# Kernel tuning notes

Measured on AMD Instinct MI355X. Metric: run time of the kernel, lower is better.

Reference implementation:

```python
import jax, jax.numpy as jnp
import numpy as np

# ---- structural constants (mirror e3nn SO3.tensor_productRs bookkeeping) ----
MUL = 2                      # multiplicity of every irrep in Rs_in / Rs_out
LS = [0, 1, 2]               # irrep orders present in Rs_in and Rs_out
L_MAX = 2                    # spherical-harmonics cutoff -> Y_dim = 9
N_BASIS, HIDDEN = 64, 64     # radial model sizes
R_MAX, GAMMA = 3.5, 4.0      # gaussian radial basis params


def _filter_paths():
    """One entry (l_filter) per (mul_out, mul_in, l_in, l_out, l_f) path."""
    paths = []
    for l_in in LS:
        for l_out in LS:
            for lf in range(abs(l_in - l_out), min(l_in + l_out, L_MAX) + 1):
                paths.extend([lf] * (MUL * MUL))  # mul_in * mul_out copies
    return paths  # len == n_path == 60


def _build_mix_matrices():
    """rf_mix[K, n_path]: broadcast each radial path weight over its 2l+1 components.
    ylm_mix[K, 9]: select Y_{l,m} for each filter component. Both 0/1, block sparse."""
    paths = _filter_paths()
    n_path = len(paths)
    K = sum(2 * l + 1 for l in paths)          # 204
    y_off = {0: 0, 1: 1, 2: 4}                 # offset of l-block inside Y (dim 9)
    rf = np.zeros((K, n_path), dtype=np.float32)
    ylm = np.zeros((K, 9), dtype=np.float32)
    k = 0
    for p, l in enumerate(paths):
        for m in range(2 * l + 1):
            rf[k, p] = 1.0
            ylm[k, y_off[l] + m] = 1.0
            k += 1
    return rf, ylm, n_path, K


def _sh_l012(n):
    """Real spherical harmonics l=0..2 on unit vectors n[Z,3] -> Y[9, Z]."""
    x, y, z = n[:, 0], n[:, 1], n[:, 2]
    c0 = 0.28209479177387814   # 1/(2 sqrt(pi))
    c1 = 0.4886025119029199    # sqrt(3/(4 pi))
    c2a = 1.0925484305920792   # sqrt(15/(4 pi))
    c2b = 0.31539156525252005  # sqrt(5/(16 pi))
    c2c = 0.5462742152960396   # sqrt(15/(16 pi))
    one = jnp.ones_like(x)
    return jnp.stack([
        c0 * one,
        c1 * y, c1 * z, c1 * x,
        c2a * x * y, c2a * y * z, c2b * (3.0 * z * z - 1.0), c2a * x * z,
        c2c * (x * x - y * y),
    ], axis=0)


def setup_inputs() -> dict:
    key = jax.random.key(0)
    k_r, k_cg, k_w1, k_w2 = jax.random.split(key, 4)
    Z = 65536
    D = MUL * sum(2 * l + 1 for l in LS)       # 18 (dim_in == dim_out)
    rf_np, ylm_np, n_path, K = _build_mix_matrices()
    r = 2.0 * jax.random.normal(k_r, (Z, 3), dtype=jnp.float32)
    cg = jax.random.normal(k_cg, (K, D, D), dtype=jnp.float32) / np.sqrt(K)
    W1 = jax.random.normal(k_w1, (N_BASIS, HIDDEN), dtype=jnp.float32) / np.sqrt(N_BASIS)
    b1 = jnp.zeros((HIDDEN,), dtype=jnp.float32)
    W2 = jax.random.normal(k_w2, (HIDDEN, n_path), dtype=jnp.float32) / np.sqrt(HIDDEN)
    b2 = jnp.zeros((n_path,), dtype=jnp.float32)
    return {"r": r, "W1": W1, "b1": b1, "W2": W2, "b2": b2,
            "cg": cg, "rf_mix": jnp.asarray(rf_np), "ylm_mix": jnp.asarray(ylm_np)}


def reference(r, W1, b1, W2, b2, cg, rf_mix, ylm_mix):
    radii = jnp.linalg.norm(r, axis=1)                    # [Z]
    n = r / (radii[:, None] + 1e-12)                      # unit directions
    Y = _sh_l012(n)                                       # [9, Z]  (sh returns [m, ...])
    centers = jnp.linspace(0.0, R_MAX, N_BASIS, dtype=jnp.float32)
    B = jnp.exp(-GAMMA * (radii[:, None] - centers) ** 2) # gaussian radial basis [Z, 64]
    R = jax.nn.relu(B @ W1 + b1) @ W2 + b2                # RadialModel -> [Z, n_path]
    Rm = jnp.einsum('kp,zp->zk', rf_mix, R)               # 'ij,zj->zi'
    Ym = jnp.einsum('ky,yz->zk', ylm_mix, Y)              # 'ij,jz->zi'
    # 'kij,zk,zk->zij' : fuse the two per-point vectors, then one GEMM over k
    kernel = jnp.einsum('kij,zk->zij', cg, Rm * Ym)       # [Z, 18, 18]
    return kernel
```

## Files before the change

### kernel.cpp

```cpp
#include <hip/hip_runtime.h>

#define NPATH 60
#define KDIM  204
#define KPAD  224
#define NIJ   324
#define NTIL  21
#define HID   64

#define BHS   88
#define CLS   232

typedef short bf16x8 __attribute__((ext_vector_type(8)));
typedef float f32x4  __attribute__((ext_vector_type(4)));

__device__ __align__(16) unsigned short g_w1s[4096];
__device__ __align__(16) unsigned short g_w2s[4096];
__device__ __align__(16) unsigned short g_cgs[75264];
__device__ unsigned char g_ptab[KDIM];
__device__ unsigned char g_ytab[KDIM];

__device__ inline unsigned short f2bf(float f) {
    unsigned int u = __builtin_bit_cast(unsigned int, f);
    u += 0x7fffu + ((u >> 16) & 1u);
    return (unsigned short)(u >> 16);
}
__device__ inline float bf2f(unsigned short h) {
    unsigned int u = ((unsigned int)h) << 16;
    return __builtin_bit_cast(float, u);
}

__global__ void prep_kernel(const float* __restrict__ W1, const float* __restrict__ W2,
                            const float* __restrict__ cg, const float* __restrict__ rf,
                            const float* __restrict__ ylm)
{
    int idx = blockIdx.x * 256 + threadIdx.x;
    if (idx < 4096) {
        int e = idx & 7, ln = (idx >> 3) & 63, nt = (idx >> 9) & 3, kc = idx >> 11;
        int k = kc * 32 + (ln >> 4) * 8 + e;
        int n = nt * 16 + (ln & 15);
        g_w1s[idx] = f2bf(W1[k * HID + n]);
    } else if (idx < 8192) {
        int j = idx - 4096;
        int e = j & 7, ln = (j >> 3) & 63, nt = (j >> 9) & 3, kc = j >> 11;
        int k = kc * 32 + (ln >> 4) * 8 + e;
        int n = nt * 16 + (ln & 15);
        g_w2s[j] = f2bf(n < NPATH ? W2[k * NPATH + n] : 0.0f);
    } else if (idx < 8192 + 75264) {
        int j = idx - 8192;
        int e = j & 7, ln = (j >> 3) & 63;
        int nt = (j >> 9) % NTIL;
        int kc = j / (512 * NTIL);
        int k = kc * 32 + (ln >> 4) * 8 + e;
        int n = nt * 16 + (ln & 15);
        g_cgs[j] = f2bf((k < KDIM && n < NIJ) ? cg[k * NIJ + n] : 0.0f);
    } else if (idx < 8192 + 75264 + KDIM) {
        int k = idx - (8192 + 75264);
        int p = 0, yy = 0;
        for (int q = 0; q < NPATH; q++) if (rf[k * NPATH + q] != 0.0f) p = q;
        for (int q = 0; q < 9; q++)     if (ylm[k * 9 + q]   != 0.0f) yy = q;
        g_ptab[k] = (unsigned char)p;
        g_ytab[k] = (unsigned char)yy;
    }
}

union SmemU {
    struct {
        unsigned short Blds[64][BHS];
        unsigned short Hlds[64][BHS];
    } p1;
    unsigned short Clds[64][CLS];
};

__global__ __launch_bounds__(256) void fused_kernel(
    const float* __restrict__ r, const float* __restrict__ b1,
    const float* __restrict__ b2, float* __restrict__ out)
{
    __shared__ SmemU sm;
    __shared__ unsigned short Rl[64][61];
    __shared__ float Yl[64][9];
    __shared__ unsigned char ptabL[KDIM];
    __shared__ unsigned char ytabL[KDIM];

    const int tid  = threadIdx.x;
    const int wv   = tid >> 6;
    const int lane = tid & 63;
    const int quad = lane >> 4;
    const int l16  = lane & 15;
    const int z0   = blockIdx.x * 64;

    for (int k = tid; k < KDIM; k += 256) {
        ptabL[k] = g_ptab[k];
        ytabL[k] = g_ytab[k];
    }
    if (tid < 64) {
        int z = z0 + tid;
        float x = r[z * 3 + 0], y = r[z * 3 + 1], zc = r[z * 3 + 2];
        float rad = sqrtf(x * x + y * y + zc * zc);
        float inv = 1.0f / (rad + 1e-12f);
        float nx = x * inv, ny = y * inv, nz = zc * inv;
        const float c0 = 0.28209479177387814f, c1 = 0.4886025119029199f;
        const float c2a = 1.0925484305920792f, c2b = 0.31539156525252005f, c2c = 0.5462742152960396f;
        Yl[tid][0] = c0;
        Yl[tid][1] = c1 * ny;
        Yl[tid][2] = c1 * nz;
        Yl[tid][3] = c1 * nx;
        Yl[tid][4] = c2a * nx * ny;
        Yl[tid][5] = c2a * ny * nz;
        Yl[tid][6] = c2b * (3.0f * nz * nz - 1.0f);
        Yl[tid][7] = c2a * nx * nz;
        Yl[tid][8] = c2c * (nx * nx - ny * ny);
    }
    {
        int zz = tid >> 2, grp = tid & 3;
        int z = z0 + zz;
        float x = r[z * 3 + 0], y = r[z * 3 + 1], zc = r[z * 3 + 2];
        float rad = sqrtf(x * x + y * y + zc * zc);
        const float step = 3.5f / 63.0f;
        const float NL2E = -5.770780163555852f;
        unsigned int* dst = (unsigned int*)&sm.p1.Blds[zz][grp * 16];
        #pragma unroll
        for (int ii = 0; ii < 8; ii++) {
            int i0 = grp * 16 + ii * 2;
            float d0 = rad - (float)i0 * step;
            float d1 = rad - (float)(i0 + 1) * step;
            unsigned int u0 = f2bf(__builtin_amdgcn_exp2f(d0 * d0 * NL2E));
            unsigned int u1 = f2bf(__builtin_amdgcn_exp2f(d1 * d1 * NL2E));
            dst[ii] = u0 | (u1 << 16);
        }
    }
    __syncthreads();

    {
        bf16x8 a0 = *(const bf16x8*)&sm.p1.Blds[wv * 16 + l16][0 + quad * 8];
        bf16x8 a1 = *(const bf16x8*)&sm.p1.Blds[wv * 16 + l16][32 + quad * 8];
        #pragma unroll
        for (int nt = 0; nt < 4; nt++) {
            bf16x8 bb0 = *(const bf16x8*)&g_w1s[((0 * 4 + nt) * 64 + lane) * 8];
            bf16x8 bb1 = *(const bf16x8*)&g_w1s[((1 * 4 + nt) * 64 + lane) * 8];
            f32x4 acc = {0.f, 0.f, 0.f, 0.f};
            acc = __builtin_amdgcn_mfma_f32_16x16x32_bf16(a0, bb0, acc, 0, 0, 0);
            acc = __builtin_amdgcn_mfma_f32_16x16x32_bf16(a1, bb1, acc, 0, 0, 0);
            int h = nt * 16 + l16;
            float bias = b1[h];
            #pragma unroll
            for (int rr = 0; rr < 4; rr++) {
                float v = acc[rr] + bias;
                v = v > 0.0f ? v : 0.0f;
                sm.p1.Hlds[wv * 16 + quad * 4 + rr][h] = f2bf(v);
            }
        }
    }
    __syncthreads();

    {
        bf16x8 a0 = *(const bf16x8*)&sm.p1.Hlds[wv * 16 + l16][0 + quad * 8];
        bf16x8 a1 = *(const bf16x8*)&sm.p1.Hlds[wv * 16 + l16][32 + quad * 8];
        #pragma unroll
        for (int nt = 0; nt < 4; nt++) {
            bf16x8 bb0 = *(const bf16x8*)&g_w2s[((0 * 4 + nt) * 64 + lane) * 8];
            bf16x8 bb1 = *(const bf16x8*)&g_w2s[((1 * 4 + nt) * 64 + lane) * 8];
            f32x4 acc = {0.f, 0.f, 0.f, 0.f};
            acc = __builtin_amdgcn_mfma_f32_16x16x32_bf16(a0, bb0, acc, 0, 0, 0);
            acc = __builtin_amdgcn_mfma_f32_16x16x32_bf16(a1, bb1, acc, 0, 0, 0);
            int p = nt * 16 + l16;
            if (p < NPATH) {
                float bias = b2[p];
                #pragma unroll
                for (int rr = 0; rr < 4; rr++)
                    Rl[wv * 16 + quad * 4 + rr][p] = f2bf(acc[rr] + bias);
            }
        }
    }
    __syncthreads();

    for (int idx = tid; idx < 64 * (KPAD / 2); idx += 256) {
        int z = idx / (KPAD / 2);
        int k = (idx % (KPAD / 2)) * 2;
        unsigned int u = 0;
        if (k < KDIM) {
            float cA = bf2f(Rl[z][ptabL[k]])     * Yl[z][ytabL[k]];
            float cB = bf2f(Rl[z][ptabL[k + 1]]) * Yl[z][ytabL[k + 1]];
            u = (unsigned int)f2bf(cA) | ((unsigned int)f2bf(cB) << 16);
        }
        *(unsigned int*)&sm.Clds[z][k] = u;
    }
    __syncthreads();

    const int ntb = wv * 5 + (wv > 0 ? 1 : 0);
    const int cnt = (wv == 0) ? 6 : 5;

    f32x4 acc[6][4];
    #pragma unroll
    for (int i = 0; i < 6; i++)
        #pragma unroll
        for (int zt = 0; zt < 4; zt++)
            acc[i][zt] = (f32x4){0.f, 0.f, 0.f, 0.f};

    #pragma unroll
    for (int kc = 0; kc < 7; kc++) {
        bf16x8 az[4];
        #pragma unroll
        for (int zt = 0; zt < 4; zt++)
            az[zt] = *(const bf16x8*)&sm.Clds[zt * 16 + l16][kc * 32 + quad * 8];

        bf16x8 bg[6];
        #pragma unroll
        for (int i = 0; i < 6; i++) {
            int nt = ntb + i; if (nt > NTIL - 1) nt = NTIL - 1;
            bg[i] = *(const bf16x8*)&g_cgs[((kc * NTIL + nt) * 64 + lane) * 8];
        }
        #pragma unroll
        for (int i = 0; i < 6; i++) {
            if (i < cnt) {
                #pragma unroll
                for (int zt = 0; zt < 4; zt++)
                    acc[i][zt] = __builtin_amdgcn_mfma_f32_16x16x32_bf16(az[zt], bg[i], acc[i][zt], 0, 0, 0);
            }
        }
    }

    #pragma unroll
    for (int i = 0; i < 6; i++) {
        if (i < cnt) {
            int col = (ntb + i) * 16 + l16;
            if (col < NIJ) {
                #pragma unroll
                for (int zt = 0; zt < 4; zt++) {
                    #pragma unroll
                    for (int rr = 0; rr < 4; rr++)
                        out[(z0 + zt * 16 + quad * 4 + rr) * NIJ + col] = acc[i][zt][rr];
                }
            }
        }
    }
}

extern "C" void kernel_launch(void* const* d_in, const int* in_sizes, int n_in,
                              void* d_out, int out_size, void* d_ws, size_t ws_size,
                              hipStream_t stream) {
    const float* r   = (const float*)d_in[0];
    const float* W1  = (const float*)d_in[1];
    const float* b1  = (const float*)d_in[2];
    const float* W2  = (const float*)d_in[3];
    const float* b2  = (const float*)d_in[4];
    const float* cg  = (const float*)d_in[5];
    const float* rf  = (const float*)d_in[6];
    const float* ylm = (const float*)d_in[7];
    float* out = (float*)d_out;

    const int Z = in_sizes[0] / 3;

    prep_kernel<<<327, 256, 0, stream>>>(W1, W2, cg, rf, ylm);
    fused_kernel<<<Z / 64, 256, 0, stream>>>(r, b1, b2, out);
}
```

Baseline: 139.4 us.

## Swizzle C tile in LDS, pack index tables, split output GEMM into halves

Packs the path and Y index tables into one 32-bit word per pair of k values. The C-building loop now gives each lane one z row and sweeps k, so the table lookups become wave-uniform. The C tile in LDS is written and read with an XOR swizzle on the byte offset to avoid bank conflicts on the bf16x8 reads. The output GEMM is split into two halves of 3 n-tiles each, which cuts live accumulator registers and lets the first half's stores overlap the second half's compute, at the cost of reloading the A fragments from LDS twice.

Measured after the change: 139.4 us. Within noise of the previous version (-0.0%).

```diff
diff --git a/kernel.cpp b/kernel.cpp
--- a/kernel.cpp
+++ b/kernel.cpp
@@ -16,8 +16,7 @@
 __device__ __align__(16) unsigned short g_w1s[4096];
 __device__ __align__(16) unsigned short g_w2s[4096];
 __device__ __align__(16) unsigned short g_cgs[75264];
-__device__ unsigned char g_ptab[KDIM];
-__device__ unsigned char g_ytab[KDIM];
+__device__ unsigned int  g_pyk[112];
 
 __device__ inline unsigned short f2bf(float f) {
     unsigned int u = __builtin_bit_cast(unsigned int, f);
@@ -53,13 +52,17 @@
         int k = kc * 32 + (ln >> 4) * 8 + e;
         int n = nt * 16 + (ln & 15);
         g_cgs[j] = f2bf((k < KDIM && n < NIJ) ? cg[k * NIJ + n] : 0.0f);
-    } else if (idx < 8192 + 75264 + KDIM) {
-        int k = idx - (8192 + 75264);
-        int p = 0, yy = 0;
-        for (int q = 0; q < NPATH; q++) if (rf[k * NPATH + q] != 0.0f) p = q;
-        for (int q = 0; q < 9; q++)     if (ylm[k * 9 + q]   != 0.0f) yy = q;
-        g_ptab[k] = (unsigned char)p;
-        g_ytab[k] = (unsigned char)yy;
+    } else if (idx < 8192 + 75264 + 112) {
+        int j = idx - (8192 + 75264);
+        int k0 = 2 * j, k1 = 2 * j + 1;
+        unsigned p0 = 0, y0 = 0, p1 = 0, y1 = 0;
+        if (k0 < KDIM) {
+            for (int q = 0; q < NPATH; q++) if (rf[k0 * NPATH + q] != 0.0f) p0 = q;
+            for (int q = 0; q < 9; q++)     if (ylm[k0 * 9 + q]   != 0.0f) y0 = q;
+            for (int q = 0; q < NPATH; q++) if (rf[k1 * NPATH + q] != 0.0f) p1 = q;
+            for (int q = 0; q < 9; q++)     if (ylm[k1 * 9 + q]   != 0.0f) y1 = q;
+        }
+        g_pyk[j] = p0 | (y0 << 8) | (p1 << 16) | (y1 << 24);
     }
 }
 
@@ -78,8 +81,7 @@
     __shared__ SmemU sm;
     __shared__ unsigned short Rl[64][61];
     __shared__ float Yl[64][9];
-    __shared__ unsigned char ptabL[KDIM];
-    __shared__ unsigned char ytabL[KDIM];
+    __shared__ unsigned int pyL[112];
 
     const int tid  = threadIdx.x;
     const int wv   = tid >> 6;
@@ -88,10 +90,7 @@
     const int l16  = lane & 15;
     const int z0   = blockIdx.x * 64;
 
-    for (int k = tid; k < KDIM; k += 256) {
-        ptabL[k] = g_ptab[k];
-        ytabL[k] = g_ytab[k];
-    }
+    if (tid < 112) pyL[tid] = g_pyk[tid];
     if (tid < 64) {
         int z = z0 + tid;
         float x = r[z * 3 + 0], y = r[z * 3 + 1], zc = r[z * 3 + 2];
@@ -173,62 +172,74 @@
     }
     __syncthreads();
 
-    for (int idx = tid; idx < 64 * (KPAD / 2); idx += 256) {
-        int z = idx / (KPAD / 2);
-        int k = (idx % (KPAD / 2)) * 2;
-        unsigned int u = 0;
-        if (k < KDIM) {
-            float cA = bf2f(Rl[z][ptabL[k]])     * Yl[z][ytabL[k]];
-            float cB = bf2f(Rl[z][ptabL[k + 1]]) * Yl[z][ytabL[k + 1]];
-            u = (unsigned int)f2bf(cA) | ((unsigned int)f2bf(cB) << 16);
-        }
-        *(unsigned int*)&sm.Clds[z][k] = u;
+    {
+        const int j0 = wv * 28;
+        char* rowp = (char*)&sm.Clds[lane][0];
+        const unsigned key = ((lane >> 3) & 3) << 4;
+        #pragma unroll
+        for (int jj = 0; jj < 28; ++jj) {
+            int j = j0 + jj;
+            int k = 2 * j;
+            unsigned u = 0;
+            if (k < KDIM) {
+                unsigned py = pyL[j];
+                float cA = bf2f(Rl[lane][py & 255])         * Yl[lane][(py >> 8) & 255];
+                float cB = bf2f(Rl[lane][(py >> 16) & 255]) * Yl[lane][(py >> 24)];
+                u = (unsigned int)f2bf(cA) | ((unsigned int)f2bf(cB) << 16);
+            }
+            *(unsigned int*)(rowp + (((unsigned)(2 * k)) ^ key)) = u;
+        }
     }
     __syncthreads();
 
     const int ntb = wv * 5 + (wv > 0 ? 1 : 0);
     const int cnt = (wv == 0) ? 6 : 5;
 
-    f32x4 acc[6][4];
     #pragma unroll
-    for (int i = 0; i < 6; i++)
-        #pragma unroll
-        for (int zt = 0; zt < 4; zt++)
-            acc[i][zt] = (f32x4){0.f, 0.f, 0.f, 0.f};
-
-    #pragma unroll
-    for (int kc = 0; kc < 7; kc++) {
-        bf16x8 az[4];
-        #pragma unroll
-        for (int zt = 0; zt < 4; zt++)
-            az[zt] = *(const bf16x8*)&sm.Clds[zt * 16 + l16][kc * 32 + quad * 8];
-
-        bf16x8 bg[6];
-        #pragma unroll
-        for (int i = 0; i < 6; i++) {
-            int nt = ntb + i; if (nt > NTIL - 1) nt = NTIL - 1;
-            bg[i] = *(const bf16x8*)&g_cgs[((kc * NTIL + nt) * 64 + lane) * 8];
-        }
-        #pragma unroll
-        for (int i = 0; i < 6; i++) {
-            if (i < cnt) {
-                #pragma unroll
-                for (int zt = 0; zt < 4; zt++)
-                    acc[i][zt] = __builtin_amdgcn_mfma_f32_16x16x32_bf16(az[zt], bg[i], acc[i][zt], 0, 0, 0);
-            }
-        }
-    }
-
-    #pragma unroll
-    for (int i = 0; i < 6; i++) {
-        if (i < cnt) {
-            int col = (ntb + i) * 16 + l16;
-            if (col < NIJ) {
-                #pragma unroll
-                for (int zt = 0; zt < 4; zt++) {
+    for (int half = 0; half < 2; half++) {
+        f32x4 acc[3][4];
+        #pragma unroll
+        for (int ii = 0; ii < 3; ii++)
+            #pragma unroll
+            for (int zt = 0; zt < 4; zt++)
+                acc[ii][zt] = (f32x4){0.f, 0.f, 0.f, 0.f};
+
+        #pragma unroll
+        for (int kc = 0; kc < 7; kc++) {
+            bf16x8 az[4];
+            #pragma unroll
+            for (int zt = 0; zt < 4; zt++) {
+                int z = zt * 16 + l16;
+                unsigned boff = ((unsigned)(kc * 64 + quad * 16)) ^ (((unsigned)((z >> 3) & 3)) << 4);
+                az[zt] = *(const bf16x8*)((const char*)&sm.Clds[z][0] + boff);
+            }
+            bf16x8 bg[3];
+            #pragma unroll
+            for (int ii = 0; ii < 3; ii++) {
+                int nt = ntb + half * 3 + ii; if (nt > NTIL - 1) nt = NTIL - 1;
+                bg[ii] = *(const bf16x8*)&g_cgs[((kc * NTIL + nt) * 64 + lane) * 8];
+            }
+            #pragma unroll
+            for (int ii = 0; ii < 3; ii++) {
+                if (half * 3 + ii < cnt) {
                     #pragma unroll
-                    for (int rr = 0; rr < 4; rr++)
-                        out[(z0 + zt * 16 + quad * 4 + rr) * NIJ + col] = acc[i][zt][rr];
+                    for (int zt = 0; zt < 4; zt++)
+                        acc[ii][zt] = __builtin_amdgcn_mfma_f32_16x16x32_bf16(az[zt], bg[ii], acc[ii][zt], 0, 0, 0);
+                }
+            }
+        }
+
+        #pragma unroll
+        for (int ii = 0; ii < 3; ii++) {
+            if (half * 3 + ii < cnt) {
+                int col = (ntb + half * 3 + ii) * 16 + l16;
+                if (col < NIJ) {
+                    #pragma unroll
+                    for (int zt = 0; zt < 4; zt++) {
+                        #pragma unroll
+                        for (int rr = 0; rr < 4; rr++)
+                            out[(z0 + zt * 16 + quad * 4 + rr) * NIJ + col] = acc[ii][zt][rr];
+                    }
                 }
             }
         }
```
